# Kernel optimization log

Measured on AMD Instinct MI355X. Metric: run time of the kernel, lower is better.

## Reference

```python
import jax, jax.numpy as jnp
import numpy as np

N_NODES = 100000
N_EDGES = 3200000


def gcn_conv(x, src, dst, ew, W, b, num_nodes):
    """PyG GCNConv: h = x@W; out[dst] += norm * h[src]; norm = d^-1/2[src]*w*d^-1/2[dst].
    src/dst/ew must already include self-loops (weight 1)."""
    h = x @ W  # [N, F_out]
    deg = jax.ops.segment_sum(ew, dst, num_segments=num_nodes)  # weighted in-degree
    dinv = jnp.where(deg > 0, jax.lax.rsqrt(deg), 0.0)
    norm = dinv[src] * ew * dinv[dst]  # [E]
    msg = h[src] * norm[:, None]  # [E, F_out] gather + scale
    out = jax.ops.segment_sum(msg, dst, num_segments=num_nodes)  # scatter-add
    return out + b


def setup_inputs() -> dict:
    key = jax.random.key(0)
    k1, k2, k3, k4, k5 = jax.random.split(key, 5)
    x = jax.random.normal(k1, (N_NODES, 35), dtype=jnp.float32)
    edge_index = jax.random.randint(k2, (2, N_EDGES), 0, N_NODES, dtype=jnp.int64)
    edge_weight = jax.random.uniform(k3, (N_EDGES,), dtype=jnp.float32)
    W1 = jax.random.normal(k4, (35, 64), dtype=jnp.float32) * (1.0 / np.sqrt(35))
    b1 = jnp.zeros((64,), dtype=jnp.float32)
    W2 = jax.random.normal(k5, (64, 2), dtype=jnp.float32) * (1.0 / np.sqrt(64))
    b2 = jnp.zeros((2,), dtype=jnp.float32)
    return {"x": x, "edge_index": edge_index, "edge_weight": edge_weight,
            "W1": W1, "b1": b1, "W2": W2, "b2": b2}


def reference(x, edge_index, edge_weight, W1, b1, W2, b2):
    n = x.shape[0]
    # add self-loops with weight 1 (PyG default fill_value=1), static shapes
    loop = jnp.arange(n, dtype=edge_index.dtype)
    src = jnp.concatenate([edge_index[0], loop])
    dst = jnp.concatenate([edge_index[1], loop])
    ew = jnp.concatenate([edge_weight, jnp.ones((n,), dtype=edge_weight.dtype)])

    h = jax.nn.relu(gcn_conv(x, src, dst, ew, W1, b1, n))
    h = gcn_conv(h, src, dst, ew, W2, b2, n)
    return jax.nn.log_softmax(h, axis=1)
```

## Files before the change

kernel.cpp:

```cpp
#include <hip/hip_runtime.h>
#include <hip/hip_fp16.h>
#include <math.h>

#define FIN 35
#define F1  64
#define BSZ 256
#define BSH 8
#define GSH 7
#define MAXNB 512
#define PCH 8192
#define SCAP 12288

__global__ void k_hist(const int* __restrict__ dst, int* __restrict__ cmat,
                       int E, int NB, int NCHUNK) {
    __shared__ int h[MAXNB];
    int c = blockIdx.x, t = threadIdx.x;
    for (int i = t; i < NB; i += 256) h[i] = 0;
    __syncthreads();
    int e0 = c * PCH, e1 = min(e0 + PCH, E);
    bool al = ((size_t)(dst + e0) & 15) == 0;
    int nv = al ? ((e1 - e0) >> 2) : 0;
    const int4* d4 = (const int4*)(dst + e0);
    for (int i = t; i < nv; i += 256) {
        int4 v = d4[i];
        atomicAdd(&h[v.x >> BSH], 1); atomicAdd(&h[v.y >> BSH], 1);
        atomicAdd(&h[v.z >> BSH], 1); atomicAdd(&h[v.w >> BSH], 1);
    }
    for (int e = e0 + (nv << 2) + t; e < e1; e += 256) atomicAdd(&h[dst[e] >> BSH], 1);
    __syncthreads();
    for (int i = t; i < NB; i += 256) cmat[(size_t)i * NCHUNK + c] = h[i];
}

__global__ void k_scan_row(int* __restrict__ cmat, int* __restrict__ rsum, int NCHUNK) {
    __shared__ int s[512];
    int b = blockIdx.x, t = threadIdx.x;
    int v = (t < NCHUNK) ? cmat[(size_t)b * NCHUNK + t] : 0;
    s[t] = v;
    __syncthreads();
    #pragma unroll
    for (int off = 1; off < 512; off <<= 1) {
        int tv = (t >= off) ? s[t - off] : 0;
        __syncthreads();
        s[t] += tv;
        __syncthreads();
    }
    if (t < NCHUNK) cmat[(size_t)b * NCHUNK + t] = s[t] - v;
    if (t == 511) rsum[b] = s[511];
}

__global__ void k_scan_buck(const int* __restrict__ rsum, int* __restrict__ bbase,
                            int* __restrict__ boff, int NB, int E) {
    __shared__ int s[1024];
    int t = threadIdx.x;
    int v = (t < NB) ? rsum[t] : 0;
    s[t] = v;
    __syncthreads();
    #pragma unroll
    for (int off = 1; off < 1024; off <<= 1) {
        int tv = (t >= off) ? s[t - off] : 0;
        __syncthreads();
        s[t] += tv;
        __syncthreads();
    }
    if (t < NB) {
        int excl = s[t] - v;
        bbase[t] = excl;
        boff[t] = excl;
    }
    if (t == 0) boff[NB] = E;
}

__global__ __launch_bounds__(512) void k_place(
        const int* __restrict__ src, const int* __restrict__ dst,
        const float* __restrict__ ew, const int* __restrict__ cmat,
        const int* __restrict__ bbase,
        int2* __restrict__ recs, int E, int NB, int NCHUNK) {
    extern __shared__ char pmem[];
    int2* lrec   = (int2*)pmem;
    int*  addr32 = (int*)(lrec + PCH);
    __shared__ int s[512];
    __shared__ int lbase[512];
    __shared__ int cur[512];
    __shared__ int gwin[512];
    int c = blockIdx.x, t = threadIdx.x;
    s[t] = 0;
    __syncthreads();
    int e0 = c * PCH, e1 = min(e0 + PCH, E);
    bool al = (((size_t)(dst + e0) | (size_t)(src + e0) | (size_t)(ew + e0)) & 15) == 0;
    int nv = al ? ((e1 - e0) >> 2) : 0;
    const int4*   s4 = (const int4*)(src + e0);
    const int4*   d4 = (const int4*)(dst + e0);
    const float4* w4 = (const float4*)(ew + e0);
    for (int i = t; i < nv; i += 512) {
        int4 v = d4[i];
        atomicAdd(&s[v.x >> BSH], 1); atomicAdd(&s[v.y >> BSH], 1);
        atomicAdd(&s[v.z >> BSH], 1); atomicAdd(&s[v.w >> BSH], 1);
    }
    for (int e = e0 + (nv << 2) + t; e < e1; e += 512) atomicAdd(&s[dst[e] >> BSH], 1);
    __syncthreads();
    int v = s[t];
    __syncthreads();
    #pragma unroll
    for (int off = 1; off < 512; off <<= 1) {
        int tv = (t >= off) ? s[t - off] : 0;
        __syncthreads();
        s[t] += tv;
        __syncthreads();
    }
    lbase[t] = s[t] - v;
    cur[t] = 0;
    gwin[t] = (t < NB) ? (cmat[(size_t)t * NCHUNK + c] + bbase[t]) : 0;
    __syncthreads();
    for (int i = t; i < nv; i += 512) {
        int4   sv = s4[i];
        int4   dv = d4[i];
        float4 wv = w4[i];
        int b, r, sl;
        b = dv.x >> BSH; r = atomicAdd(&cur[b], 1); sl = lbase[b] + r;
        lrec[sl] = make_int2(sv.x | ((dv.x & (BSZ-1)) << 24), __float_as_int(wv.x));
        addr32[sl] = gwin[b] + r;
        b = dv.y >> BSH; r = atomicAdd(&cur[b], 1); sl = lbase[b] + r;
        lrec[sl] = make_int2(sv.y | ((dv.y & (BSZ-1)) << 24), __float_as_int(wv.y));
        addr32[sl] = gwin[b] + r;
        b = dv.z >> BSH; r = atomicAdd(&cur[b], 1); sl = lbase[b] + r;
        lrec[sl] = make_int2(sv.z | ((dv.z & (BSZ-1)) << 24), __float_as_int(wv.z));
        addr32[sl] = gwin[b] + r;
        b = dv.w >> BSH; r = atomicAdd(&cur[b], 1); sl = lbase[b] + r;
        lrec[sl] = make_int2(sv.w | ((dv.w & (BSZ-1)) << 24), __float_as_int(wv.w));
        addr32[sl] = gwin[b] + r;
    }
    for (int e = e0 + (nv << 2) + t; e < e1; e += 512) {
        int d = dst[e];
        int b = d >> BSH;
        int r = atomicAdd(&cur[b], 1);
        int sl = lbase[b] + r;
        lrec[sl] = make_int2(src[e] | ((d & (BSZ-1)) << 24), __float_as_int(ew[e]));
        addr32[sl] = gwin[b] + r;
    }
    __syncthreads();
    int cnt = e1 - e0;
    for (int i = t; i < cnt; i += 512) recs[addr32[i]] = lrec[i];
}

__global__ __launch_bounds__(512) void k_sort(
        const int* __restrict__ boff, const int2* __restrict__ recs_in,
        int2* __restrict__ recs_out, int* __restrict__ row_ptr,
        float* __restrict__ dinv, int n) {
    extern __shared__ unsigned short inv16[];
    __shared__ int   hcnt[BSZ];
    __shared__ int   hoff[BSZ];
    __shared__ float dsum[BSZ];
    int b = blockIdx.x, t = threadIdx.x;
    if (t < BSZ) { hcnt[t] = 0; dsum[t] = 1.0f; }
    __syncthreads();
    int s0 = boff[b], s1 = boff[b + 1];
    int cnt = s1 - s0;
    for (int i = t; i < cnt; i += 512) {
        int2 rc = recs_in[s0 + i];
        int dl = ((unsigned)rc.x) >> 24;
        atomicAdd(&hcnt[dl], 1);
        atomicAdd(&dsum[dl], __int_as_float(rc.y));
    }
    __syncthreads();
    int v = 0;
    if (t < BSZ) { v = hcnt[t]; hoff[t] = v; }
    __syncthreads();
    #pragma unroll
    for (int off = 1; off < BSZ; off <<= 1) {
        int tv = 0;
        if (t < BSZ && t >= off) tv = hoff[t - off];
        __syncthreads();
        if (t < BSZ) hoff[t] += tv;
        __syncthreads();
    }
    if (t < BSZ) {
        int excl = hoff[t] - v;
        int node = b * BSZ + t;
        if (node < n) {
            row_ptr[node] = s0 + excl;
            dinv[node] = rsqrtf(dsum[t]);
            if (node == n - 1) row_ptr[n] = s1;
        }
        hcnt[t] = excl;
    }
    __syncthreads();
    if (cnt <= SCAP) {
        for (int i = t; i < cnt; i += 512) {
            int2 rc = recs_in[s0 + i];
            int dl = ((unsigned)rc.x) >> 24;
            int pos = atomicAdd(&hcnt[dl], 1);
            inv16[pos] = (unsigned short)i;
        }
        __syncthreads();
        for (int o = t; o < cnt; o += 512) {
            int2 rc = recs_in[s0 + inv16[o]];
            recs_out[s0 + o] = make_int2((rc.x & 0xFFFFFF) << GSH, rc.y);
        }
    } else {
        for (int i = t; i < cnt; i += 512) {
            int2 rc = recs_in[s0 + i];
            int dl = ((unsigned)rc.x) >> 24;
            int pos = atomicAdd(&hcnt[dl], 1);
            recs_out[s0 + pos] = make_int2((rc.x & 0xFFFFFF) << GSH, rc.y);
        }
    }
}

__global__ void k_gemm1(const float* __restrict__ x, const float* __restrict__ W1,
                        const float* __restrict__ dinv, __half* __restrict__ g1, int n) {
    __shared__ float W1s[FIN * F1];
    __shared__ float xs[64 * FIN];
    int t = threadIdx.x;
    for (int i = t; i < (FIN * F1) / 4; i += 256) ((float4*)W1s)[i] = ((const float4*)W1)[i];
    int row0 = blockIdx.x * 64;
    int nrows = min(64, n - row0);
    const float* xbase = x + (size_t)row0 * FIN;
    int tot = nrows * FIN;
    int totv = tot >> 2;
    for (int i = t; i < totv; i += 256) ((float4*)xs)[i] = ((const float4*)xbase)[i];
    for (int i = (totv << 2) + t; i < tot; i += 256) xs[i] = xbase[i];
    __syncthreads();
    int wave = t >> 6, f = t & 63;
    for (int rl = wave; rl < nrows; rl += 4) {
        float acc = 0.0f;
        #pragma unroll
        for (int k = 0; k < FIN; k++) acc += xs[rl * FIN + k] * W1s[k * F1 + f];
        int row = row0 + rl;
        g1[(size_t)row * F1 + f] = __float2half(acc * dinv[row]);
    }
}

__global__ void k_gather1(const int* __restrict__ rp, const int2* __restrict__ csr,
                          const __half* __restrict__ g1,
                          const float* __restrict__ dinv, const float* __restrict__ b1,
                          const float* __restrict__ W2, float* __restrict__ g2, int n) {
    int wid = (int)((blockIdx.x * (long long)blockDim.x + threadIdx.x) >> 6);
    int f = threadIdx.x & 63;
    if (wid >= n) return;
    const char* g1b = (const char*)g1 + f * 2;
    int start = rp[wid], end = rp[wid + 1];
    float acc = 0.0f;
    int e = start;
    for (; e + 16 <= end; e += 16) {
        float a[16];
        int2 r[16];
        #pragma unroll
        for (int j = 0; j < 16; j++) r[j] = csr[e + j];
        #pragma unroll
        for (int j = 0; j < 16; j++)
            a[j] = __half2float(*(const __half*)(g1b + (unsigned)r[j].x));
        #pragma unroll
        for (int j = 0; j < 16; j++) acc += __int_as_float(r[j].y) * a[j];
    }
    for (; e + 4 <= end; e += 4) {
        int2 r0 = csr[e], r1 = csr[e+1], r2 = csr[e+2], r3 = csr[e+3];
        float a0 = __half2float(*(const __half*)(g1b + (unsigned)r0.x));
        float a1 = __half2float(*(const __half*)(g1b + (unsigned)r1.x));
        float a2 = __half2float(*(const __half*)(g1b + (unsigned)r2.x));
        float a3 = __half2float(*(const __half*)(g1b + (unsigned)r3.x));
        acc += __int_as_float(r0.y) * a0; acc += __int_as_float(r1.y) * a1;
        acc += __int_as_float(r2.y) * a2; acc += __int_as_float(r3.y) * a3;
    }
    for (; e < end; e++) {
        int2 r = csr[e];
        acc += __int_as_float(r.y) * __half2float(*(const __half*)(g1b + (unsigned)r.x));
    }
    float dv = dinv[wid];
    float h = dv * (acc + __half2float(g1[(size_t)wid * F1 + f])) + b1[f];
    h = h > 0.0f ? h : 0.0f;
    float2 w2v = ((const float2*)W2)[f];
    float z0 = h * w2v.x, z1 = h * w2v.y;
    #pragma unroll
    for (int off = 32; off > 0; off >>= 1) {
        z0 += __shfl_xor(z0, off, 64);
        z1 += __shfl_xor(z1, off, 64);
    }
    if (f == 0) {
        g2[(size_t)wid * 2 + 0] = dv * z0;
        g2[(size_t)wid * 2 + 1] = dv * z1;
    }
}

__global__ void k_gather2(const int* __restrict__ rp, const int2* __restrict__ csr,
                          const float* __restrict__ g2,
                          const float* __restrict__ dinv, const float* __restrict__ b2,
                          float* __restrict__ out, int n) {
    int w = (int)((blockIdx.x * (long long)blockDim.x + threadIdx.x) >> 6);
    int lane = threadIdx.x & 63;
    int half = lane >> 5, sub = lane & 31;
    int node = w * 2 + half;
    if (node >= n) return;
    const char* g2b = (const char*)g2;
    int start = rp[node], end = rp[node + 1];
    float a0 = 0.0f, a1 = 0.0f;
    int e = start + sub;
    for (; e + 96 < end; e += 128) {
        int2 q0 = csr[e], q1 = csr[e + 32], q2 = csr[e + 64], q3 = csr[e + 96];
        float2 v0 = *(const float2*)(g2b + (((unsigned)q0.x) >> 4));
        float2 v1 = *(const float2*)(g2b + (((unsigned)q1.x) >> 4));
        float2 v2 = *(const float2*)(g2b + (((unsigned)q2.x) >> 4));
        float2 v3 = *(const float2*)(g2b + (((unsigned)q3.x) >> 4));
        a0 += __int_as_float(q0.y) * v0.x; a1 += __int_as_float(q0.y) * v0.y;
        a0 += __int_as_float(q1.y) * v1.x; a1 += __int_as_float(q1.y) * v1.y;
        a0 += __int_as_float(q2.y) * v2.x; a1 += __int_as_float(q2.y) * v2.y;
        a0 += __int_as_float(q3.y) * v3.x; a1 += __int_as_float(q3.y) * v3.y;
    }
    for (; e < end; e += 32) {
        int2 r = csr[e];
        float wt = __int_as_float(r.y);
        float2 gv = *(const float2*)(g2b + (((unsigned)r.x) >> 4));
        a0 += wt * gv.x; a1 += wt * gv.y;
    }
    #pragma unroll
    for (int off = 16; off > 0; off >>= 1) {
        a0 += __shfl_xor(a0, off, 64);
        a1 += __shfl_xor(a1, off, 64);
    }
    if (sub == 0) {
        float dv = dinv[node];
        float2 sv = ((const float2*)g2)[node];
        float z0 = dv * (a0 + sv.x) + b2[0];
        float z1 = dv * (a1 + sv.y) + b2[1];
        float m = fmaxf(z0, z1);
        float lse = m + logf(expf(z0 - m) + expf(z1 - m));
        ((float2*)out)[node] = make_float2(z0 - lse, z1 - lse);
    }
}

extern "C" void kernel_launch(void* const* d_in, const int* in_sizes, int n_in,
                              void* d_out, int out_size, void* d_ws, size_t ws_size,
                              hipStream_t stream) {
    const float* x  = (const float*)d_in[0];
    const int*   ei = (const int*)d_in[1];
    const float* ew = (const float*)d_in[2];
    const float* W1 = (const float*)d_in[3];
    const float* b1 = (const float*)d_in[4];
    const float* W2 = (const float*)d_in[5];
    const float* b2 = (const float*)d_in[6];
    float* out = (float*)d_out;

    int n = in_sizes[0] / FIN;
    int E = in_sizes[2];
    const int* src = ei;
    const int* dst = ei + E;
    int NB = (n + BSZ - 1) / BSZ;
    int NCHUNK = (E + PCH - 1) / PCH;
    int M = NB * NCHUNK;

    char* ws = (char*)d_ws;
    size_t off = 0;
    auto alloc = [&](size_t bytes) -> void* {
        void* p = ws + off;
        off += (bytes + 15) & ~(size_t)15;
        return p;
    };
    int*    cmat    = (int*)   alloc((size_t)M * 4);
    int*    rsum    = (int*)   alloc((size_t)NB * 4);
    int*    bbase   = (int*)   alloc((size_t)NB * 4);
    int*    boff    = (int*)   alloc((size_t)(NB + 1) * 4);
    int*    row_ptr = (int*)   alloc((size_t)(n + 1) * 4);
    float*  dinv    = (float*) alloc((size_t)n * 4);
    int2*   recs_a  = (int2*)  alloc((size_t)E * 8);
    int2*   recs_b  = (int2*)  alloc((size_t)E * 8);
    __half* g1      = (__half*)alloc((size_t)n * F1 * 2);
    float*  g2      = (float*) alloc((size_t)n * 2 * 4);

    size_t place_lds = (size_t)PCH * 8 + (size_t)PCH * 4;
    size_t sort_lds  = (size_t)SCAP * 2;

    int g2_waves = (n + 1) / 2 + 1;

    k_hist     <<<NCHUNK, 256, 0, stream>>>(dst, cmat, E, NB, NCHUNK);
    k_scan_row <<<NB, 512, 0, stream>>>(cmat, rsum, NCHUNK);
    k_scan_buck<<<1, 1024, 0, stream>>>(rsum, bbase, boff, NB, E);
    k_place    <<<NCHUNK, 512, place_lds, stream>>>(src, dst, ew, cmat, bbase, recs_a, E, NB, NCHUNK);
    k_sort     <<<NB, 512, sort_lds, stream>>>(boff, recs_a, recs_b, row_ptr, dinv, n);
    k_gemm1    <<<(n + 63) / 64, 256, 0, stream>>>(x, W1, dinv, g1, n);
    k_gather1  <<<(n + 3) / 4, 256, 0, stream>>>(row_ptr, recs_b, g1, dinv, b1, W2, g2, n);
    k_gather2  <<<(g2_waves + 3) / 4, 256, 0, stream>>>(row_ptr, recs_b, g2, dinv, b2, out, n);
}
```

Baseline: 297.3 us.

## Fuse bucket scan into row scan and GEMM1 into sort kernel

Merges the single-block bucket scan into the per-row scan kernel using a last-block-done atomic counter, which removes one launch at the cost of a memset. Fuses the x@W1 GEMM into the bucket sort kernel, so each 256-node bucket block computes its own g1 rows with dinv taken from shared memory instead of global. Moves the src<<GSH shift from the sort into the placement stage. This removes two kernel launches and one dinv reload, but raises LDS use per sort block (W1 and a 256x35 x tile), which may lower occupancy. NB must also stay at or below 512 for the fused scan.

```diff
diff --git a/kernel.cpp b/kernel.cpp
--- a/kernel.cpp
+++ b/kernel.cpp
@@ -31,8 +31,12 @@
     for (int i = t; i < NB; i += 256) cmat[(size_t)i * NCHUNK + c] = h[i];
 }
 
-__global__ void k_scan_row(int* __restrict__ cmat, int* __restrict__ rsum, int NCHUNK) {
+__global__ __launch_bounds__(512) void k_scan_rows(
+        int* __restrict__ cmat, int* __restrict__ rsum,
+        int* __restrict__ bbase, int* __restrict__ boff,
+        int* __restrict__ done, int NB, int NCHUNK, int E) {
     __shared__ int s[512];
+    __shared__ int is_last;
     int b = blockIdx.x, t = threadIdx.x;
     int v = (t < NCHUNK) ? cmat[(size_t)b * NCHUNK + t] : 0;
     s[t] = v;
@@ -46,24 +50,25 @@
     }
     if (t < NCHUNK) cmat[(size_t)b * NCHUNK + t] = s[t] - v;
     if (t == 511) rsum[b] = s[511];
-}
-
-__global__ void k_scan_buck(const int* __restrict__ rsum, int* __restrict__ bbase,
-                            int* __restrict__ boff, int NB, int E) {
-    __shared__ int s[1024];
-    int t = threadIdx.x;
-    int v = (t < NB) ? rsum[t] : 0;
-    s[t] = v;
-    __syncthreads();
-    #pragma unroll
-    for (int off = 1; off < 1024; off <<= 1) {
+    if (t == 0) {
+        __threadfence();
+        is_last = (atomicAdd(done, 1) == gridDim.x - 1);
+    }
+    __syncthreads();
+    if (!is_last) return;
+    __threadfence();
+    int rv = (t < NB) ? rsum[t] : 0;
+    s[t] = rv;
+    __syncthreads();
+    #pragma unroll
+    for (int off = 1; off < 512; off <<= 1) {
         int tv = (t >= off) ? s[t - off] : 0;
         __syncthreads();
         s[t] += tv;
         __syncthreads();
     }
     if (t < NB) {
-        int excl = s[t] - v;
+        int excl = s[t] - rv;
         bbase[t] = excl;
         boff[t] = excl;
     }
@@ -117,16 +122,16 @@
         float4 wv = w4[i];
         int b, r, sl;
         b = dv.x >> BSH; r = atomicAdd(&cur[b], 1); sl = lbase[b] + r;
-        lrec[sl] = make_int2(sv.x | ((dv.x & (BSZ-1)) << 24), __float_as_int(wv.x));
+        lrec[sl] = make_int2((sv.x << GSH) | ((dv.x & (BSZ-1)) << 24), __float_as_int(wv.x));
         addr32[sl] = gwin[b] + r;
         b = dv.y >> BSH; r = atomicAdd(&cur[b], 1); sl = lbase[b] + r;
-        lrec[sl] = make_int2(sv.y | ((dv.y & (BSZ-1)) << 24), __float_as_int(wv.y));
+        lrec[sl] = make_int2((sv.y << GSH) | ((dv.y & (BSZ-1)) << 24), __float_as_int(wv.y));
         addr32[sl] = gwin[b] + r;
         b = dv.z >> BSH; r = atomicAdd(&cur[b], 1); sl = lbase[b] + r;
-        lrec[sl] = make_int2(sv.z | ((dv.z & (BSZ-1)) << 24), __float_as_int(wv.z));
+        lrec[sl] = make_int2((sv.z << GSH) | ((dv.z & (BSZ-1)) << 24), __float_as_int(wv.z));
         addr32[sl] = gwin[b] + r;
         b = dv.w >> BSH; r = atomicAdd(&cur[b], 1); sl = lbase[b] + r;
-        lrec[sl] = make_int2(sv.w | ((dv.w & (BSZ-1)) << 24), __float_as_int(wv.w));
+        lrec[sl] = make_int2((sv.w << GSH) | ((dv.w & (BSZ-1)) << 24), __float_as_int(wv.w));
         addr32[sl] = gwin[b] + r;
     }
     for (int e = e0 + (nv << 2) + t; e < e1; e += 512) {
@@ -134,7 +139,7 @@
         int b = d >> BSH;
         int r = atomicAdd(&cur[b], 1);
         int sl = lbase[b] + r;
-        lrec[sl] = make_int2(src[e] | ((d & (BSZ-1)) << 24), __float_as_int(ew[e]));
+        lrec[sl] = make_int2((src[e] << GSH) | ((d & (BSZ-1)) << 24), __float_as_int(ew[e]));
         addr32[sl] = gwin[b] + r;
     }
     __syncthreads();
@@ -142,16 +147,27 @@
     for (int i = t; i < cnt; i += 512) recs[addr32[i]] = lrec[i];
 }
 
-__global__ __launch_bounds__(512) void k_sort(
+__global__ __launch_bounds__(512) void k_sortg(
         const int* __restrict__ boff, const int2* __restrict__ recs_in,
         int2* __restrict__ recs_out, int* __restrict__ row_ptr,
-        float* __restrict__ dinv, int n) {
+        float* __restrict__ dinv, const float* __restrict__ x,
+        const float* __restrict__ W1, __half* __restrict__ g1, int n) {
     extern __shared__ unsigned short inv16[];
+    __shared__ float W1s[FIN * F1];
+    __shared__ float xs[BSZ * FIN];
     __shared__ int   hcnt[BSZ];
     __shared__ int   hoff[BSZ];
     __shared__ float dsum[BSZ];
     int b = blockIdx.x, t = threadIdx.x;
     if (t < BSZ) { hcnt[t] = 0; dsum[t] = 1.0f; }
+    for (int i = t; i < (FIN * F1) / 4; i += 512) ((float4*)W1s)[i] = ((const float4*)W1)[i];
+    int node0 = b * BSZ;
+    int nrows = min(BSZ, n - node0);
+    const float* xbase = x + (size_t)node0 * FIN;
+    int tot = nrows * FIN;
+    int totv = tot >> 2;
+    for (int i = t; i < totv; i += 512) ((float4*)xs)[i] = ((const float4*)xbase)[i];
+    for (int i = (totv << 2) + t; i < tot; i += 512) xs[i] = xbase[i];
     __syncthreads();
     int s0 = boff[b], s1 = boff[b + 1];
     int cnt = s1 - s0;
@@ -175,10 +191,12 @@
     }
     if (t < BSZ) {
         int excl = hoff[t] - v;
-        int node = b * BSZ + t;
+        int node = node0 + t;
         if (node < n) {
             row_ptr[node] = s0 + excl;
-            dinv[node] = rsqrtf(dsum[t]);
+            float dv = rsqrtf(dsum[t]);
+            dinv[node] = dv;
+            dsum[t] = dv;
             if (node == n - 1) row_ptr[n] = s1;
         }
         hcnt[t] = excl;
@@ -194,39 +212,22 @@
         __syncthreads();
         for (int o = t; o < cnt; o += 512) {
             int2 rc = recs_in[s0 + inv16[o]];
-            recs_out[s0 + o] = make_int2((rc.x & 0xFFFFFF) << GSH, rc.y);
+            recs_out[s0 + o] = make_int2(rc.x & 0xFFFFFF, rc.y);
         }
     } else {
         for (int i = t; i < cnt; i += 512) {
             int2 rc = recs_in[s0 + i];
             int dl = ((unsigned)rc.x) >> 24;
             int pos = atomicAdd(&hcnt[dl], 1);
-            recs_out[s0 + pos] = make_int2((rc.x & 0xFFFFFF) << GSH, rc.y);
+            recs_out[s0 + pos] = make_int2(rc.x & 0xFFFFFF, rc.y);
         }
     }
-}
-
-__global__ void k_gemm1(const float* __restrict__ x, const float* __restrict__ W1,
-                        const float* __restrict__ dinv, __half* __restrict__ g1, int n) {
-    __shared__ float W1s[FIN * F1];
-    __shared__ float xs[64 * FIN];
-    int t = threadIdx.x;
-    for (int i = t; i < (FIN * F1) / 4; i += 256) ((float4*)W1s)[i] = ((const float4*)W1)[i];
-    int row0 = blockIdx.x * 64;
-    int nrows = min(64, n - row0);
-    const float* xbase = x + (size_t)row0 * FIN;
-    int tot = nrows * FIN;
-    int totv = tot >> 2;
-    for (int i = t; i < totv; i += 256) ((float4*)xs)[i] = ((const float4*)xbase)[i];
-    for (int i = (totv << 2) + t; i < tot; i += 256) xs[i] = xbase[i];
-    __syncthreads();
     int wave = t >> 6, f = t & 63;
-    for (int rl = wave; rl < nrows; rl += 4) {
+    for (int rl = wave; rl < nrows; rl += 8) {
         float acc = 0.0f;
         #pragma unroll
         for (int k = 0; k < FIN; k++) acc += xs[rl * FIN + k] * W1s[k * F1 + f];
-        int row = row0 + rl;
-        g1[(size_t)row * F1 + f] = __float2half(acc * dinv[row]);
+        g1[(size_t)(node0 + rl) * F1 + f] = __float2half(acc * dsum[rl]);
     }
 }
 
@@ -354,6 +355,7 @@
         off += (bytes + 15) & ~(size_t)15;
         return p;
     };
+    int*    done    = (int*)   alloc(16);
     int*    cmat    = (int*)   alloc((size_t)M * 4);
     int*    rsum    = (int*)   alloc((size_t)NB * 4);
     int*    bbase   = (int*)   alloc((size_t)NB * 4);
@@ -366,16 +368,15 @@
     float*  g2      = (float*) alloc((size_t)n * 2 * 4);
 
     size_t place_lds = (size_t)PCH * 8 + (size_t)PCH * 4;
-    size_t sort_lds  = (size_t)SCAP * 2;
+    size_t sortg_lds = (size_t)SCAP * 2;
 
     int g2_waves = (n + 1) / 2 + 1;
 
-    k_hist     <<<NCHUNK, 256, 0, stream>>>(dst, cmat, E, NB, NCHUNK);
-    k_scan_row <<<NB, 512, 0, stream>>>(cmat, rsum, NCHUNK);
-    k_scan_buck<<<1, 1024, 0, stream>>>(rsum, bbase, boff, NB, E);
-    k_place    <<<NCHUNK, 512, place_lds, stream>>>(src, dst, ew, cmat, bbase, recs_a, E, NB, NCHUNK);
-    k_sort     <<<NB, 512, sort_lds, stream>>>(boff, recs_a, recs_b, row_ptr, dinv, n);
-    k_gemm1    <<<(n + 63) / 64, 256, 0, stream>>>(x, W1, dinv, g1, n);
-    k_gather1  <<<(n + 3) / 4, 256, 0, stream>>>(row_ptr, recs_b, g1, dinv, b1, W2, g2, n);
-    k_gather2  <<<(g2_waves + 3) / 4, 256, 0, stream>>>(row_ptr, recs_b, g2, dinv, b2, out, n);
-}
+    hipMemsetAsync(done, 0, 4, stream);
+    k_hist      <<<NCHUNK, 256, 0, stream>>>(dst, cmat, E, NB, NCHUNK);
+    k_scan_rows <<<NB, 512, 0, stream>>>(cmat, rsum, bbase, boff, done, NB, NCHUNK, E);
+    k_place     <<<NCHUNK, 512, place_lds, stream>>>(src, dst, ew, cmat, bbase, recs_a, E, NB, NCHUNK);
+    k_sortg     <<<NB, 512, sortg_lds, stream>>>(boff, recs_a, recs_b, row_ptr, dinv, x, W1, g1, n);
+    k_gather1   <<<(n + 3) / 4, 256, 0, stream>>>(row_ptr, recs_b, g1, dinv, b1, W2, g2, n);
+    k_gather2   <<<(g2_waves + 3) / 4, 256, 0, stream>>>(row_ptr, recs_b, g2, dinv, b2, out, n);
+}
```

Measured after the change: 302.8 us. Within noise of the previous version (+1.8%).
